# Performance work log

Hardware: AMD Instinct MI355X
Metric: run time of the kernel (lower is better)

The kernel has to match this reference:

```python
import jax, jax.numpy as jnp
import numpy as np

N_NODES = 100000
N_EDGES = 1600000
IN_DIM = 256
HEADS = 4
OUT_DIM = 32
ALPHA = 0.2  # leaky relu slope


def setup_inputs() -> dict:
    key = jax.random.key(0)
    k1, k2, k3, k4, k5, k6 = jax.random.split(key, 6)
    feature = jax.random.normal(k1, (N_NODES, IN_DIM), dtype=jnp.float32)
    src = jax.random.randint(k2, (N_EDGES,), 0, N_NODES, dtype=jnp.int32)
    dst = jax.random.randint(k3, (N_EDGES,), 0, N_NODES, dtype=jnp.int32)
    W_fc = jax.random.normal(k4, (IN_DIM, HEADS * OUT_DIM), dtype=jnp.float32) * 0.05
    attn_l = jax.random.normal(k5, (1, HEADS, OUT_DIM), dtype=jnp.float32) * 0.1
    attn_r = jax.random.normal(k6, (1, HEADS, OUT_DIM), dtype=jnp.float32) * 0.1
    return {"feature": feature, "src": src, "dst": dst, "W_fc": W_fc,
            "attn_l": attn_l, "attn_r": attn_r}


def reference(feature, src, dst, W_fc, attn_l, attn_r):
    # node projection: [N, H, D]
    ft = (feature @ W_fc).reshape(feature.shape[0], HEADS, OUT_DIM)
    # per-node attention scores: [N, H]
    a1 = jnp.sum(ft * attn_l, axis=-1)
    a2 = jnp.sum(ft * attn_r, axis=-1)
    # edge attention logits: gather src/dst + leaky relu -> [E, H]
    e = a1[src] + a2[dst]
    e = jnp.where(e > 0, e, ALPHA * e)
    # segment softmax over destination groups
    n = feature.shape[0]
    e_max = jax.ops.segment_max(e, dst, num_segments=n)  # [N, H]
    e_exp = jnp.exp(e - e_max[dst])
    e_sum = jax.ops.segment_sum(e_exp, dst, num_segments=n)  # [N, H]
    alpha = e_exp / e_sum[dst]  # [E, H]
    # weighted scatter-sum aggregation: [N, H, D]
    msgs = ft[src] * alpha[:, :, None]
    out = jax.ops.segment_sum(msgs, dst, num_segments=n)
    return out
```

## Files before the change

### kernel.cpp

```cpp
#include <hip/hip_runtime.h>
#include <hip/hip_fp16.h>

#define N_NODES 100000
#define N_EDGES 1600000
#define IN_DIM 256
#define HEADS 4
#define OUT_DIM 32
#define NHD 128
#define LEAKY 0.2f

#define SCAN_BLOCK 1024
#define N_SCAN_BLOCKS ((N_NODES + SCAN_BLOCK - 1) / SCAN_BLOCK)

__global__ void init_kernel(int* __restrict__ deg) {
    int i = blockIdx.x * blockDim.x + threadIdx.x;
    if (i < N_NODES) deg[i] = 0;
}

__launch_bounds__(256, 2)
__global__ void gemm_kernel(const float* __restrict__ feature,
                            const float* __restrict__ W,
                            const float* __restrict__ attn_l,
                            const float* __restrict__ attn_r,
                            __half* __restrict__ ft,
                            float* __restrict__ a1,
                            float* __restrict__ a2) {
    __shared__ float sA[32][132];
    __shared__ float sW[32][132];
    const int t  = threadIdx.x;
    const int tx = t & 15;
    const int ty = t >> 4;
    const int nb = blockIdx.x * 128;

    float acc[8][8];
#pragma unroll
    for (int i = 0; i < 8; ++i)
#pragma unroll
        for (int j = 0; j < 8; ++j) acc[i][j] = 0.f;

    for (int kt = 0; kt < 8; ++kt) {
        __syncthreads();
#pragma unroll
        for (int p = 0; p < 4; ++p) {
            int idx  = t + p * 256;
            int row  = idx >> 3;
            int c4   = idx & 7;
            int node = nb + row;
            float4 v = make_float4(0.f, 0.f, 0.f, 0.f);
            if (node < N_NODES)
                v = *(const float4*)&feature[(size_t)node * IN_DIM + kt * 32 + c4 * 4];
            sA[c4 * 4 + 0][row] = v.x;
            sA[c4 * 4 + 1][row] = v.y;
            sA[c4 * 4 + 2][row] = v.z;
            sA[c4 * 4 + 3][row] = v.w;
        }
#pragma unroll
        for (int p = 0; p < 4; ++p) {
            int idx = t + p * 256;
            int row = idx >> 5;
            int c4  = idx & 31;
            float4 v = *(const float4*)&W[(size_t)(kt * 32 + row) * NHD + c4 * 4];
            *(float4*)&sW[row][c4 * 4] = v;
        }
        __syncthreads();

#pragma unroll 8
        for (int k = 0; k < 32; ++k) {
            float4 a0  = *(const float4*)&sA[k][ty * 8];
            float4 a1v = *(const float4*)&sA[k][ty * 8 + 4];
            float4 b0  = *(const float4*)&sW[k][tx * 8];
            float4 b1  = *(const float4*)&sW[k][tx * 8 + 4];
            float a[8] = {a0.x, a0.y, a0.z, a0.w, a1v.x, a1v.y, a1v.z, a1v.w};
            float b[8] = {b0.x, b0.y, b0.z, b0.w, b1.x, b1.y, b1.z, b1.w};
#pragma unroll
            for (int i = 0; i < 8; ++i)
#pragma unroll
                for (int j = 0; j < 8; ++j)
                    acc[i][j] = fmaf(a[i], b[j], acc[i][j]);
        }
    }

    float al[8], ar[8];
#pragma unroll
    for (int j = 0; j < 8; ++j) {
        al[j] = attn_l[tx * 8 + j];
        ar[j] = attn_r[tx * 8 + j];
    }

#pragma unroll
    for (int i = 0; i < 8; ++i) {
        int node = nb + ty * 8 + i;
        if (node < N_NODES) {
            __half2 pack[4];
            pack[0] = __floats2half2_rn(acc[i][0], acc[i][1]);
            pack[1] = __floats2half2_rn(acc[i][2], acc[i][3]);
            pack[2] = __floats2half2_rn(acc[i][4], acc[i][5]);
            pack[3] = __floats2half2_rn(acc[i][6], acc[i][7]);
            *(float4*)&ft[(size_t)node * NHD + tx * 8] = *(float4*)pack;
        }
        float pl = 0.f, pr = 0.f;
#pragma unroll
        for (int j = 0; j < 8; ++j) {
            pl = fmaf(acc[i][j], al[j], pl);
            pr = fmaf(acc[i][j], ar[j], pr);
        }
        pl += __shfl_xor(pl, 1); pl += __shfl_xor(pl, 2);
        pr += __shfl_xor(pr, 1); pr += __shfl_xor(pr, 2);
        if ((tx & 3) == 0 && node < N_NODES) {
            a1[node * HEADS + (tx >> 2)] = pl;
            a2[node * HEADS + (tx >> 2)] = pr;
        }
    }
}

__global__ void hist_kernel(const int* __restrict__ dst, int* __restrict__ deg,
                            int* __restrict__ edge_pos) {
    int i = blockIdx.x * blockDim.x + threadIdx.x;
    if (i < N_EDGES) edge_pos[i] = atomicAdd(&deg[dst[i]], 1);
}

__global__ void scan1_kernel(const int* __restrict__ deg,
                             int* __restrict__ partial,
                             int* __restrict__ blocksum) {
    __shared__ int wsum[16];
    const int tid  = threadIdx.x;
    const int lane = tid & 63;
    const int wid  = tid >> 6;
    const int i    = blockIdx.x * SCAN_BLOCK + tid;
    int v = (i < N_NODES) ? deg[i] : 0;
    int x = v;
#pragma unroll
    for (int o = 1; o < 64; o <<= 1) {
        int y = __shfl_up(x, o);
        if (lane >= o) x += y;
    }
    if (lane == 63) wsum[wid] = x;
    __syncthreads();
    if (wid == 0 && lane < 16) {
        int w = wsum[lane];
#pragma unroll
        for (int o = 1; o < 16; o <<= 1) {
            int y = __shfl_up(w, o);
            if (lane >= o) w += y;
        }
        wsum[lane] = w;
    }
    __syncthreads();
    int woff = (wid > 0) ? wsum[wid - 1] : 0;
    if (i < N_NODES) partial[i] = woff + x - v;
    if (tid == SCAN_BLOCK - 1) blocksum[blockIdx.x] = wsum[15];
}

__global__ void scan2_kernel(const int* __restrict__ blocksum,
                             int* __restrict__ blockoff,
                             int* __restrict__ offsets) {
    __shared__ int wtot[2];
    const int tid  = threadIdx.x;
    const int lane = tid & 63;
    const int wid  = tid >> 6;
    int v = (tid < N_SCAN_BLOCKS) ? blocksum[tid] : 0;
    int x = v;
#pragma unroll
    for (int o = 1; o < 64; o <<= 1) {
        int y = __shfl_up(x, o);
        if (lane >= o) x += y;
    }
    if (lane == 63) wtot[wid] = x;
    __syncthreads();
    int add = (wid == 1) ? wtot[0] : 0;
    if (tid < N_SCAN_BLOCKS) blockoff[tid] = add + x - v;
    if (tid == N_SCAN_BLOCKS - 1) offsets[N_NODES] = add + x;
}

__global__ void scan3_kernel(const int* __restrict__ partial,
                             const int* __restrict__ blockoff,
                             int* __restrict__ offsets) {
    int i = blockIdx.x * SCAN_BLOCK + threadIdx.x;
    if (i < N_NODES) offsets[i] = partial[i] + blockoff[blockIdx.x];
}

__global__ void fill_kernel(const int* __restrict__ src, const int* __restrict__ dst,
                            const int* __restrict__ offsets,
                            const int* __restrict__ edge_pos,
                            int* __restrict__ src_sorted) {
    int i = blockIdx.x * blockDim.x + threadIdx.x;
    if (i < N_EDGES) {
        int idx = offsets[dst[i]] + edge_pos[i];
        src_sorted[idx] = src[i];
    }
}

__launch_bounds__(256)
__global__ void agg_kernel(const __half* __restrict__ ft,
                           const float* __restrict__ a1,
                           const float* __restrict__ a2,
                           const int* __restrict__ offsets,
                           const int* __restrict__ src_sorted,
                           float* __restrict__ out) {
    const int wave = threadIdx.x >> 6;
    const int lane = threadIdx.x & 63;
    const int node = blockIdx.x * 4 + wave;
    if (node >= N_NODES) return;
    const int h = lane >> 4;

    const float a2v = a2[node * HEADS + h];
    const int e0 = offsets[node];
    const int e1 = offsets[node + 1];

    float accx = 0.f, accy = 0.f, wsum = 0.f;
    int e = e0;

    for (; e + 3 < e1; e += 4) {
        int s0 = src_sorted[e];
        int s1 = src_sorted[e + 1];
        int s2 = src_sorted[e + 2];
        int s3 = src_sorted[e + 3];
        float b0 = a1[s0 * HEADS + h];
        float b1 = a1[s1 * HEADS + h];
        float b2 = a1[s2 * HEADS + h];
        float b3 = a1[s3 * HEADS + h];
        __half2 h0 = *(const __half2*)&ft[(size_t)s0 * NHD + lane * 2];
        __half2 h1 = *(const __half2*)&ft[(size_t)s1 * NHD + lane * 2];
        __half2 h2 = *(const __half2*)&ft[(size_t)s2 * NHD + lane * 2];
        __half2 h3 = *(const __half2*)&ft[(size_t)s3 * NHD + lane * 2];
        float2 v0 = __half22float2(h0);
        float2 v1 = __half22float2(h1);
        float2 v2 = __half22float2(h2);
        float2 v3 = __half22float2(h3);
        float ev0 = b0 + a2v; ev0 = ev0 > 0.f ? ev0 : LEAKY * ev0;
        float ev1 = b1 + a2v; ev1 = ev1 > 0.f ? ev1 : LEAKY * ev1;
        float ev2 = b2 + a2v; ev2 = ev2 > 0.f ? ev2 : LEAKY * ev2;
        float ev3 = b3 + a2v; ev3 = ev3 > 0.f ? ev3 : LEAKY * ev3;
        float w0 = __expf(ev0), w1 = __expf(ev1), w2 = __expf(ev2), w3 = __expf(ev3);
        accx = fmaf(w0, v0.x, accx); accy = fmaf(w0, v0.y, accy);
        accx = fmaf(w1, v1.x, accx); accy = fmaf(w1, v1.y, accy);
        accx = fmaf(w2, v2.x, accx); accy = fmaf(w2, v2.y, accy);
        accx = fmaf(w3, v3.x, accx); accy = fmaf(w3, v3.y, accy);
        wsum += w0 + w1 + w2 + w3;
    }
    for (; e < e1; ++e) {
        int s    = src_sorted[e];
        float ev = a1[s * HEADS + h] + a2v;
        ev       = ev > 0.f ? ev : LEAKY * ev;
        float w  = __expf(ev);
        float2 v = __half22float2(*(const __half2*)&ft[(size_t)s * NHD + lane * 2]);
        accx = fmaf(w, v.x, accx);
        accy = fmaf(w, v.y, accy);
        wsum += w;
    }
    float inv = (e1 > e0) ? 1.f / wsum : 0.f;
    float2 o = make_float2(accx * inv, accy * inv);
    *(float2*)&out[(size_t)node * NHD + lane * 2] = o;
}

extern "C" void kernel_launch(void* const* d_in, const int* in_sizes, int n_in,
                              void* d_out, int out_size, void* d_ws, size_t ws_size,
                              hipStream_t stream) {
    const float* feature = (const float*)d_in[0];
    const int*   src     = (const int*)d_in[1];
    const int*   dst     = (const int*)d_in[2];
    const float* W       = (const float*)d_in[3];
    const float* attn_l  = (const float*)d_in[4];
    const float* attn_r  = (const float*)d_in[5];
    float*       out     = (float*)d_out;

    char* ws = (char*)d_ws;
    size_t off = 0;
    auto alloc = [&](size_t bytes) -> void* {
        void* p = ws + off;
        off = (off + bytes + 255) & ~(size_t)255;
        return p;
    };
    __half* ft        = (__half*)alloc((size_t)N_NODES * NHD * 2);
    float* a1         = (float*)alloc((size_t)N_NODES * HEADS * 4);
    float* a2         = (float*)alloc((size_t)N_NODES * HEADS * 4);
    int*   deg        = (int*)alloc((size_t)N_NODES * 4);
    int*   offsets    = (int*)alloc((size_t)(N_NODES + 1) * 4);
    int*   src_sorted = (int*)alloc((size_t)N_EDGES * 4);
    int*   edge_pos   = (int*)alloc((size_t)N_EDGES * 4);
    int*   partial    = (int*)alloc((size_t)N_NODES * 4);
    int*   blocksum   = (int*)alloc((size_t)N_SCAN_BLOCKS * 4);
    int*   blockoff   = (int*)alloc((size_t)N_SCAN_BLOCKS * 4);

    init_kernel<<<(N_NODES + 255) / 256, 256, 0, stream>>>(deg);
    gemm_kernel<<<(N_NODES + 127) / 128, 256, 0, stream>>>(feature, W, attn_l, attn_r, ft, a1, a2);
    hist_kernel<<<(N_EDGES + 255) / 256, 256, 0, stream>>>(dst, deg, edge_pos);
    scan1_kernel<<<N_SCAN_BLOCKS, SCAN_BLOCK, 0, stream>>>(deg, partial, blocksum);
    scan2_kernel<<<1, 128, 0, stream>>>(blocksum, blockoff, offsets);
    scan3_kernel<<<N_SCAN_BLOCKS, SCAN_BLOCK, 0, stream>>>(partial, blockoff, offsets);
    fill_kernel<<<(N_EDGES + 255) / 256, 256, 0, stream>>>(src, dst, offsets, edge_pos, src_sorted);
    agg_kernel<<<(N_NODES + 3) / 4, 256, 0, stream>>>(ft, a1, a2, offsets, src_sorted, out);
}
```

Before: 427.9 us.

## Use fp16 MFMA with split hi/lo weights for node projection GEMM

Replaces the scalar FP32 FMA GEMM for the node projection with MFMA 16x16x32 fp16 matrix instructions. A new prep kernel transposes W and splits it into fp16 high and low parts so the weight side keeps near-fp32 precision, while features are rounded to fp16. Launch bounds are raised to allow more waves per CU. The aim is to cut the compute-bound cost of the GEMM, in exchange for an extra small kernel launch and reduced precision on the feature operand.

```diff
diff --git a/kernel.cpp b/kernel.cpp
--- a/kernel.cpp
+++ b/kernel.cpp
@@ -12,103 +12,136 @@
 #define SCAN_BLOCK 1024
 #define N_SCAN_BLOCKS ((N_NODES + SCAN_BLOCK - 1) / SCAN_BLOCK)
 
+typedef _Float16 f16x8 __attribute__((ext_vector_type(8)));
+typedef _Float16 f16x4 __attribute__((ext_vector_type(4)));
+typedef float    f32x4 __attribute__((ext_vector_type(4)));
+
 __global__ void init_kernel(int* __restrict__ deg) {
     int i = blockIdx.x * blockDim.x + threadIdx.x;
     if (i < N_NODES) deg[i] = 0;
 }
 
-__launch_bounds__(256, 2)
+__global__ void wprep_kernel(const float* __restrict__ W,
+                             _Float16* __restrict__ Wt_hi,
+                             _Float16* __restrict__ Wt_lo) {
+    int i = blockIdx.x * blockDim.x + threadIdx.x;
+    if (i < NHD * IN_DIM) {
+        int c = i >> 8;
+        int k = i & 255;
+        float w = W[(size_t)k * NHD + c];
+        _Float16 hi = (_Float16)w;
+        _Float16 lo = (_Float16)(w - (float)hi);
+        Wt_hi[i] = hi;
+        Wt_lo[i] = lo;
+    }
+}
+
+__launch_bounds__(256, 4)
 __global__ void gemm_kernel(const float* __restrict__ feature,
-                            const float* __restrict__ W,
+                            const _Float16* __restrict__ Wt_hi,
+                            const _Float16* __restrict__ Wt_lo,
                             const float* __restrict__ attn_l,
                             const float* __restrict__ attn_r,
                             __half* __restrict__ ft,
                             float* __restrict__ a1,
                             float* __restrict__ a2) {
-    __shared__ float sA[32][132];
-    __shared__ float sW[32][132];
-    const int t  = threadIdx.x;
-    const int tx = t & 15;
-    const int ty = t >> 4;
-    const int nb = blockIdx.x * 128;
-
-    float acc[8][8];
-#pragma unroll
-    for (int i = 0; i < 8; ++i)
-#pragma unroll
-        for (int j = 0; j < 8; ++j) acc[i][j] = 0.f;
+    __shared__ _Float16 sA [128][40];
+    __shared__ _Float16 sWh[128][40];
+    __shared__ _Float16 sWl[128][40];
+
+    const int t    = threadIdx.x;
+    const int w    = t >> 6;
+    const int lane = t & 63;
+    const int l15  = lane & 15;
+    const int kg   = lane >> 4;
+    const int nb   = blockIdx.x * 128;
+
+    f32x4 acc[8][2];
+#pragma unroll
+    for (int nt = 0; nt < 8; ++nt) {
+        acc[nt][0] = (f32x4){0.f, 0.f, 0.f, 0.f};
+        acc[nt][1] = (f32x4){0.f, 0.f, 0.f, 0.f};
+    }
 
     for (int kt = 0; kt < 8; ++kt) {
         __syncthreads();
 #pragma unroll
         for (int p = 0; p < 4; ++p) {
             int idx  = t + p * 256;
-            int row  = idx >> 3;
+            int node = idx >> 3;
             int c4   = idx & 7;
-            int node = nb + row;
             float4 v = make_float4(0.f, 0.f, 0.f, 0.f);
-            if (node < N_NODES)
-                v = *(const float4*)&feature[(size_t)node * IN_DIM + kt * 32 + c4 * 4];
-            sA[c4 * 4 + 0][row] = v.x;
-            sA[c4 * 4 + 1][row] = v.y;
-            sA[c4 * 4 + 2][row] = v.z;
-            sA[c4 * 4 + 3][row] = v.w;
-        }
-#pragma unroll
-        for (int p = 0; p < 4; ++p) {
-            int idx = t + p * 256;
-            int row = idx >> 5;
-            int c4  = idx & 31;
-            float4 v = *(const float4*)&W[(size_t)(kt * 32 + row) * NHD + c4 * 4];
-            *(float4*)&sW[row][c4 * 4] = v;
+            if (nb + node < N_NODES)
+                v = *(const float4*)&feature[(size_t)(nb + node) * IN_DIM + kt * 32 + c4 * 4];
+            f16x4 h;
+            h[0] = (_Float16)v.x; h[1] = (_Float16)v.y;
+            h[2] = (_Float16)v.z; h[3] = (_Float16)v.w;
+            *(f16x4*)&sA[node][c4 * 4] = h;
+        }
+#pragma unroll
+        for (int p = 0; p < 2; ++p) {
+            int c   = t + p * 256;
+            int col = c >> 2;
+            int kc  = c & 3;
+            *(f16x8*)&sWh[col][kc * 8] =
+                *(const f16x8*)&Wt_hi[(size_t)col * IN_DIM + kt * 32 + kc * 8];
+            *(f16x8*)&sWl[col][kc * 8] =
+                *(const f16x8*)&Wt_lo[(size_t)col * IN_DIM + kt * 32 + kc * 8];
         }
         __syncthreads();
 
-#pragma unroll 8
-        for (int k = 0; k < 32; ++k) {
-            float4 a0  = *(const float4*)&sA[k][ty * 8];
-            float4 a1v = *(const float4*)&sA[k][ty * 8 + 4];
-            float4 b0  = *(const float4*)&sW[k][tx * 8];
-            float4 b1  = *(const float4*)&sW[k][tx * 8 + 4];
-            float a[8] = {a0.x, a0.y, a0.z, a0.w, a1v.x, a1v.y, a1v.z, a1v.w};
-            float b[8] = {b0.x, b0.y, b0.z, b0.w, b1.x, b1.y, b1.z, b1.w};
-#pragma unroll
-            for (int i = 0; i < 8; ++i)
-#pragma unroll
-                for (int j = 0; j < 8; ++j)
-                    acc[i][j] = fmaf(a[i], b[j], acc[i][j]);
-        }
-    }
-
-    float al[8], ar[8];
-#pragma unroll
-    for (int j = 0; j < 8; ++j) {
-        al[j] = attn_l[tx * 8 + j];
-        ar[j] = attn_r[tx * 8 + j];
-    }
-
-#pragma unroll
-    for (int i = 0; i < 8; ++i) {
-        int node = nb + ty * 8 + i;
-        if (node < N_NODES) {
-            __half2 pack[4];
-            pack[0] = __floats2half2_rn(acc[i][0], acc[i][1]);
-            pack[1] = __floats2half2_rn(acc[i][2], acc[i][3]);
-            pack[2] = __floats2half2_rn(acc[i][4], acc[i][5]);
-            pack[3] = __floats2half2_rn(acc[i][6], acc[i][7]);
-            *(float4*)&ft[(size_t)node * NHD + tx * 8] = *(float4*)pack;
+        f16x8 wh0 = *(const f16x8*)&sWh[w * 32 + l15][kg * 8];
+        f16x8 wh1 = *(const f16x8*)&sWh[w * 32 + 16 + l15][kg * 8];
+        f16x8 wl0 = *(const f16x8*)&sWl[w * 32 + l15][kg * 8];
+        f16x8 wl1 = *(const f16x8*)&sWl[w * 32 + 16 + l15][kg * 8];
+
+#pragma unroll
+        for (int nt = 0; nt < 8; ++nt) {
+            f16x8 af = *(const f16x8*)&sA[nt * 16 + l15][kg * 8];
+            acc[nt][0] = __builtin_amdgcn_mfma_f32_16x16x32_f16(wh0, af, acc[nt][0], 0, 0, 0);
+            acc[nt][0] = __builtin_amdgcn_mfma_f32_16x16x32_f16(wl0, af, acc[nt][0], 0, 0, 0);
+            acc[nt][1] = __builtin_amdgcn_mfma_f32_16x16x32_f16(wh1, af, acc[nt][1], 0, 0, 0);
+            acc[nt][1] = __builtin_amdgcn_mfma_f32_16x16x32_f16(wl1, af, acc[nt][1], 0, 0, 0);
+        }
+    }
+
+    float al8[8], ar8[8];
+#pragma unroll
+    for (int ct = 0; ct < 2; ++ct)
+#pragma unroll
+        for (int r = 0; r < 4; ++r) {
+            int cb = ct * 16 + kg * 4 + r;
+            al8[ct * 4 + r] = attn_l[w * 32 + cb];
+            ar8[ct * 4 + r] = attn_r[w * 32 + cb];
+        }
+
+#pragma unroll
+    for (int nt = 0; nt < 8; ++nt) {
+        int node = nb + nt * 16 + l15;
+        bool valid = node < N_NODES;
+        if (valid) {
+            f16x4 s0, s1;
+#pragma unroll
+            for (int r = 0; r < 4; ++r) {
+                s0[r] = (_Float16)acc[nt][0][r];
+                s1[r] = (_Float16)acc[nt][1][r];
+            }
+            *(f16x4*)&ft[(size_t)node * NHD + w * 32 + kg * 4]      = s0;
+            *(f16x4*)&ft[(size_t)node * NHD + w * 32 + 16 + kg * 4] = s1;
         }
         float pl = 0.f, pr = 0.f;
 #pragma unroll
-        for (int j = 0; j < 8; ++j) {
-            pl = fmaf(acc[i][j], al[j], pl);
-            pr = fmaf(acc[i][j], ar[j], pr);
-        }
-        pl += __shfl_xor(pl, 1); pl += __shfl_xor(pl, 2);
-        pr += __shfl_xor(pr, 1); pr += __shfl_xor(pr, 2);
-        if ((tx & 3) == 0 && node < N_NODES) {
-            a1[node * HEADS + (tx >> 2)] = pl;
-            a2[node * HEADS + (tx >> 2)] = pr;
+        for (int ct = 0; ct < 2; ++ct)
+#pragma unroll
+            for (int r = 0; r < 4; ++r) {
+                pl = fmaf(acc[nt][ct][r], al8[ct * 4 + r], pl);
+                pr = fmaf(acc[nt][ct][r], ar8[ct * 4 + r], pr);
+            }
+        pl += __shfl_xor(pl, 16); pl += __shfl_xor(pl, 32);
+        pr += __shfl_xor(pr, 16); pr += __shfl_xor(pr, 32);
+        if (kg == 0 && valid) {
+            a1[node * HEADS + w] = pl;
+            a2[node * HEADS + w] = pr;
         }
     }
 }
@@ -271,19 +304,23 @@
         off = (off + bytes + 255) & ~(size_t)255;
         return p;
     };
-    __half* ft        = (__half*)alloc((size_t)N_NODES * NHD * 2);
-    float* a1         = (float*)alloc((size_t)N_NODES * HEADS * 4);
-    float* a2         = (float*)alloc((size_t)N_NODES * HEADS * 4);
-    int*   deg        = (int*)alloc((size_t)N_NODES * 4);
-    int*   offsets    = (int*)alloc((size_t)(N_NODES + 1) * 4);
-    int*   src_sorted = (int*)alloc((size_t)N_EDGES * 4);
-    int*   edge_pos   = (int*)alloc((size_t)N_EDGES * 4);
-    int*   partial    = (int*)alloc((size_t)N_NODES * 4);
-    int*   blocksum   = (int*)alloc((size_t)N_SCAN_BLOCKS * 4);
-    int*   blockoff   = (int*)alloc((size_t)N_SCAN_BLOCKS * 4);
+    __half*    ft        = (__half*)alloc((size_t)N_NODES * NHD * 2);
+    float*     a1        = (float*)alloc((size_t)N_NODES * HEADS * 4);
+    float*     a2        = (float*)alloc((size_t)N_NODES * HEADS * 4);
+    int*       deg       = (int*)alloc((size_t)N_NODES * 4);
+    int*       offsets   = (int*)alloc((size_t)(N_NODES + 1) * 4);
+    int*       src_sorted= (int*)alloc((size_t)N_EDGES * 4);
+    int*       edge_pos  = (int*)alloc((size_t)N_EDGES * 4);
+    int*       partial   = (int*)alloc((size_t)N_NODES * 4);
+    int*       blocksum  = (int*)alloc((size_t)N_SCAN_BLOCKS * 4);
+    int*       blockoff  = (int*)alloc((size_t)N_SCAN_BLOCKS * 4);
+    _Float16*  Wt_hi     = (_Float16*)alloc((size_t)NHD * IN_DIM * 2);
+    _Float16*  Wt_lo     = (_Float16*)alloc((size_t)NHD * IN_DIM * 2);
 
     init_kernel<<<(N_NODES + 255) / 256, 256, 0, stream>>>(deg);
-    gemm_kernel<<<(N_NODES + 127) / 128, 256, 0, stream>>>(feature, W, attn_l, attn_r, ft, a1, a2);
+    wprep_kernel<<<(NHD * IN_DIM + 255) / 256, 256, 0, stream>>>(W, Wt_hi, Wt_lo);
+    gemm_kernel<<<(N_NODES + 127) / 128, 256, 0, stream>>>(feature, Wt_hi, Wt_lo,
+                                                           attn_l, attn_r, ft, a1, a2);
     hist_kernel<<<(N_EDGES + 255) / 256, 256, 0, stream>>>(dst, deg, edge_pos);
     scan1_kernel<<<N_SCAN_BLOCKS, SCAN_BLOCK, 0, stream>>>(deg, partial, blocksum);
     scan2_kernel<<<1, 128, 0, stream>>>(blocksum, blockoff, offsets);
```

Result: faster. 391.6 us (-8.5%).
